# Kernel tuning notes

Measured on AMD Instinct MI355X. Metric: run time of the kernel, lower is better.

Reference implementation:

```python
import jax, jax.numpy as jnp
import numpy as np

B = 8192   # batch
N = 1024   # input feature dim
D = 64     # rotation dimension
K = D * (D - 1) // 2  # 2016 upper-triangular entries


def setup_inputs() -> dict:
    key = jax.random.key(0)
    k1, k2 = jax.random.split(key, 2)
    x = jax.random.normal(k1, (B, N), dtype=jnp.float32)
    # nn.Linear(N, K) parameters (kaiming-uniform-ish scale)
    W = jax.random.normal(k2, (K, N), dtype=jnp.float32) / np.float32(np.sqrt(N))
    b = jnp.zeros((K,), dtype=jnp.float32)
    return {"x": x, "W": W, "b": b}


def _skew_expm(A):
    # A is real skew-symmetric => iA is Hermitian: iA = V diag(w) V^H, w real.
    # Hence expm(A) = V diag(exp(-i w)) V^H, which is real orthogonal.
    # Mathematically identical to torch.linalg.matrix_exp(A).
    w, V = jnp.linalg.eigh(1j * A)              # complex64 eigh, batched
    R = jnp.einsum('bij,bj,bkj->bik', V, jnp.exp(-1j * w), V.conj())
    return jnp.real(R)


def reference(x, W, b):
    v = jax.nn.silu(x) @ W.T + b                # (B, K)
    iu, ju = jnp.triu_indices(D, k=1)           # strict upper triangle
    A = jnp.zeros((x.shape[0], D, D), v.dtype)
    A = A.at[:, iu, ju].set(v)
    A = A.at[:, ju, iu].set(-v)                 # skew-symmetric
    return _skew_expm(A)                        # (B, D, D)
```

## Files before the change

### kernel.cpp

```cpp
#include <hip/hip_runtime.h>
#include <hip/hip_bf16.h>
#include <hip/hip_fp16.h>
#include <math.h>

#define BB 8192
#define NF 1024
#define KKc 2016
#define DD 64

typedef unsigned short u16;
typedef __attribute__((ext_vector_type(4))) float f32x4;
typedef __attribute__((ext_vector_type(4))) unsigned int u32x4;
typedef __attribute__((ext_vector_type(8))) short s16x8;
typedef __attribute__((ext_vector_type(8))) _Float16 f16x8;
typedef __attribute__((ext_vector_type(8))) unsigned short u16x8;

union BF2U { __hip_bfloat162 b; unsigned u; };
union H2U { __half2 h; unsigned u; };
union F16U { s16x8 s; f16x8 h; };

__device__ __forceinline__ unsigned pk_hi(float a, float b, float& fa, float& fb) {
  BF2U r; r.b = __float22bfloat162_rn(make_float2(a, b));
  float2 f = __bfloat1622float2(r.b);
  fa = f.x; fb = f.y;
  return r.u;
}
__device__ __forceinline__ unsigned pk(float a, float b) {
  BF2U r; r.b = __float22bfloat162_rn(make_float2(a, b));
  return r.u;
}
__device__ __forceinline__ unsigned pkh(float a, float b) {
  H2U r; r.h = __float22half2_rn(make_float2(a, b));
  return r.u;
}

__device__ __forceinline__ void split4(const float t0, const float t1, const float t2,
                                       const float t3, uint2& h, uint2& l) {
  float f0, f1, f2, f3;
  h.x = pk_hi(t0, t1, f0, f1);
  h.y = pk_hi(t2, t3, f2, f3);
  l.x = pk(t0 - f0, t1 - f1);
  l.y = pk(t2 - f2, t3 - f3);
}

__global__ __launch_bounds__(256)
void silu_f16_kernel(const float* __restrict__ x, u16* __restrict__ xf) {
  const int idx = blockIdx.x * 256 + threadIdx.x;
  float4 vv = ((const float4*)x)[idx];
  float a[4] = {vv.x, vv.y, vv.z, vv.w};
#pragma unroll
  for (int i = 0; i < 4; i++) a[i] = a[i] / (1.f + __expf(-a[i]));
  uint2 o;
  o.x = pkh(a[0], a[1]);
  o.y = pkh(a[2], a[3]);
  ((uint2*)xf)[idx] = o;
}

__global__ __launch_bounds__(256)
void w_f16_kernel(const float* __restrict__ W, u16* __restrict__ wfp) {
  const int idx = blockIdx.x * 256 + threadIdx.x;
  const int row = idx >> 8;
  float4 vv = make_float4(0.f, 0.f, 0.f, 0.f);
  if (row < KKc) vv = ((const float4*)W)[idx];
  uint2 o;
  o.x = pkh(vv.x, vv.y);
  o.y = pkh(vv.z, vv.w);
  ((uint2*)wfp)[idx] = o;
}

typedef __attribute__((address_space(1))) const unsigned int gu32;
typedef __attribute__((address_space(3))) unsigned int lu32;

__device__ __forceinline__ void gload_lds16(const void* g, void* l) {
  __builtin_amdgcn_global_load_lds((gu32*)g, (lu32*)l, 16, 0, 0);
}

__device__ __forceinline__ s16x8 frag_row32(const u16* T, int row, int kc) {
  const int c = kc ^ ((row >> 1) & 3);
  return *(const s16x8*)(T + row * 32 + c * 8);
}

__global__ __launch_bounds__(256, 4)
void gemm_f16_kernel(const u16* __restrict__ xf, const u16* __restrict__ wfp,
                     const float* __restrict__ bias, float* __restrict__ v) {
  __shared__ __align__(16) u16 Af[128 * 32];
  __shared__ __align__(16) u16 Bf[128 * 32];
  const int tid = threadIdx.x;
  const int l = tid & 63, w = tid >> 6;
  const int wi = w >> 1, wj = w & 1;
  const int lin = (blockIdx.x & 7) * 128 + (blockIdx.x >> 3);
  const int n0 = (lin & 15) * 128;
  const int m0 = (lin >> 4) * 128;
  const int kc = l >> 4, lr = l & 15;

  const u16* P = (w < 2) ? xf : wfp;
  u16* T = (w < 2) ? Af : Bf;
  const int row0 = ((w < 2) ? m0 : n0) + (w & 1) * 64;
  u16* Th = T + (w & 1) * 2048;

  f32x4 acc[4][4];
  const f32x4 zz = {0.f, 0.f, 0.f, 0.f};
#pragma unroll
  for (int a = 0; a < 4; a++)
#pragma unroll
    for (int b = 0; b < 4; b++) acc[a][b] = zz;

  for (int k0 = 0; k0 < NF; k0 += 32) {
#pragma unroll
    for (int c4 = 0; c4 < 4; c4++) {
      const int slot = c4 * 64 + l;
      const int r = slot >> 2;
      const int c = (slot & 3) ^ ((r >> 1) & 3);
      gload_lds16(P + (size_t)(row0 + r) * NF + k0 + c * 8, Th + c4 * 512);
    }
    __syncthreads();

    F16U fa[4], fb[4];
#pragma unroll
    for (int a = 0; a < 4; a++) fa[a].s = frag_row32(Af, wi * 64 + a * 16 + lr, kc);
#pragma unroll
    for (int b = 0; b < 4; b++) fb[b].s = frag_row32(Bf, wj * 64 + b * 16 + lr, kc);
#pragma unroll
    for (int b = 0; b < 4; b++)
#pragma unroll
      for (int a = 0; a < 4; a++)
        acc[a][b] = __builtin_amdgcn_mfma_f32_16x16x32_f16(fa[a].h, fb[b].h, acc[a][b], 0, 0, 0);
    __syncthreads();
  }

  const int grp = l >> 4;
#pragma unroll
  for (int b = 0; b < 4; b++) {
    const int n = n0 + wj * 64 + b * 16 + lr;
    if (n < KKc) {
      const float bb = bias[n];
#pragma unroll
      for (int a = 0; a < 4; a++) {
        const int mbase = m0 + wi * 64 + a * 16 + grp * 4;
#pragma unroll
        for (int i = 0; i < 4; i++)
          v[(size_t)(mbase + i) * KKc + n] = acc[a][b][i] + bb;
      }
    }
  }
}

#define BM 128
#define BN 128
#define BKr 16
#define XST 132

__global__ __launch_bounds__(256, 2)
void gemm_silu_kernel(const float* __restrict__ x, const float* __restrict__ W,
                      const float* __restrict__ bias, float* __restrict__ v) {
  __shared__ float xs[BKr * XST];
  __shared__ float wl[BKr * XST];
  const int tid = threadIdx.x;
  const int tx = tid & 15, ty = tid >> 4;
  const int c0g = blockIdx.x * BN;
  const int m0 = blockIdx.y * BM;
  const int lrow = tid >> 2;
  const int lu = (tid & 3) << 2;

  float acc[2][2][4][4];
#pragma unroll
  for (int a = 0; a < 2; a++)
#pragma unroll
    for (int b = 0; b < 2; b++)
#pragma unroll
      for (int i = 0; i < 4; i++)
#pragma unroll
        for (int j = 0; j < 4; j++) acc[a][b][i][j] = 0.f;

  for (int n0 = 0; n0 < NF; n0 += BKr) {
#pragma unroll
    for (int p = 0; p < 2; p++) {
      const int row = lrow + 64 * p;
      float4 xv = *(const float4*)(x + (size_t)(m0 + row) * NF + n0 + lu);
      float xa[4] = {xv.x, xv.y, xv.z, xv.w};
#pragma unroll
      for (int u = 0; u < 4; u++) {
        const float val = xa[u];
        xs[(lu + u) * XST + row] = val / (1.f + __expf(-val));
      }
      const int wr = c0g + row;
      float4 wv = make_float4(0.f, 0.f, 0.f, 0.f);
      if (wr < KKc) wv = *(const float4*)(W + (size_t)wr * NF + n0 + lu);
      float wa[4] = {wv.x, wv.y, wv.z, wv.w};
#pragma unroll
      for (int u = 0; u < 4; u++) wl[(lu + u) * XST + row] = wa[u];
    }
    __syncthreads();
#pragma unroll
    for (int k0 = 0; k0 < BKr; k0 += 4) {
#pragma unroll
      for (int kk = 0; kk < 4; kk++) {
        const float* xr = xs + (k0 + kk) * XST;
        const float* wr_ = wl + (k0 + kk) * XST;
        float4 t;
        t = *(const float4*)(xr + 4 * ty);       float a0[4] = {t.x, t.y, t.z, t.w};
        t = *(const float4*)(xr + 64 + 4 * ty);  float a1[4] = {t.x, t.y, t.z, t.w};
        t = *(const float4*)(wr_ + 4 * tx);      float b0[4] = {t.x, t.y, t.z, t.w};
        t = *(const float4*)(wr_ + 64 + 4 * tx); float b1[4] = {t.x, t.y, t.z, t.w};
#pragma unroll
        for (int i = 0; i < 4; i++)
#pragma unroll
          for (int j = 0; j < 4; j++) {
            acc[0][0][i][j] = fmaf(a0[i], b0[j], acc[0][0][i][j]);
            acc[0][1][i][j] = fmaf(a0[i], b1[j], acc[0][1][i][j]);
            acc[1][0][i][j] = fmaf(a1[i], b0[j], acc[1][0][i][j]);
            acc[1][1][i][j] = fmaf(a1[i], b1[j], acc[1][1][i][j]);
          }
      }
    }
    __syncthreads();
  }
#pragma unroll
  for (int rb = 0; rb < 2; rb++)
#pragma unroll
    for (int ii = 0; ii < 4; ii++) {
      const int row = m0 + rb * 64 + 4 * ty + ii;
#pragma unroll
      for (int cb = 0; cb < 2; cb++) {
        const int c = c0g + cb * 64 + 4 * tx;
        if (c < KKc) {
          float4 bb = *(const float4*)(bias + c);
          float4 o;
          o.x = acc[rb][cb][ii][0] + bb.x;
          o.y = acc[rb][cb][ii][1] + bb.y;
          o.z = acc[rb][cb][ii][2] + bb.z;
          o.w = acc[rb][cb][ii][3] + bb.w;
          *(float4*)(v + (size_t)row * KKc + c) = o;
        }
      }
    }
}


__device__ __forceinline__ s16x8 fragld(const u16* P, int row, int chunk) {
  return *(const s16x8*)(P + ((row << 6) | ((chunk ^ (row & 7)) << 3)));
}

__device__ __forceinline__ void mat_mm3(const u16* APh, const u16* APl,
                                        const u16* BPh, const u16* BPl,
                                        f32x4 acc[2][2], int wi, int wj, int g, int lr) {
#pragma unroll
  for (int kb = 0; kb < 2; kb++) {
    const int ch = (kb << 2) | g;
    s16x8 bh[2], bl[2];
#pragma unroll
    for (int b = 0; b < 2; b++) {
      const int n = wj * 32 + b * 16 + lr;
      bh[b] = fragld(BPh, n, ch);
      bl[b] = fragld(BPl, n, ch);
    }
#pragma unroll
    for (int a = 0; a < 2; a++) {
      const int r = wi * 32 + a * 16 + lr;
      const s16x8 ah = fragld(APh, r, ch);
      const s16x8 al = fragld(APl, r, ch);
#pragma unroll
      for (int b = 0; b < 2; b++) {
        acc[a][b] = __builtin_amdgcn_mfma_f32_16x16x32_bf16(ah, bh[b], acc[a][b], 0, 0, 0);
        acc[a][b] = __builtin_amdgcn_mfma_f32_16x16x32_bf16(ah, bl[b], acc[a][b], 0, 0, 0);
        acc[a][b] = __builtin_amdgcn_mfma_f32_16x16x32_bf16(al, bh[b], acc[a][b], 0, 0, 0);
      }
    }
  }
}

__device__ __forceinline__ void mat_mm1h(const u16* AP, const u16* BP,
                                         f32x4 acc[2][2], int wi, int wj, int g, int lr) {
#pragma unroll
  for (int kb = 0; kb < 2; kb++) {
    const int ch = (kb << 2) | g;
    F16U bh[2];
#pragma unroll
    for (int b = 0; b < 2; b++) bh[b].s = fragld(BP, wj * 32 + b * 16 + lr, ch);
#pragma unroll
    for (int a = 0; a < 2; a++) {
      F16U ah; ah.s = fragld(AP, wi * 32 + a * 16 + lr, ch);
#pragma unroll
      for (int b = 0; b < 2; b++)
        acc[a][b] = __builtin_amdgcn_mfma_f32_16x16x32_f16(ah.h, bh[b].h, acc[a][b], 0, 0, 0);
    }
  }
}

__device__ __forceinline__ void pack_col(u16* Ch, u16* Cl, const f32x4 acc[2][2],
                                         int wi, int wj, int g, int lr) {
#pragma unroll
  for (int a = 0; a < 2; a++) {
    const int r0 = wi * 32 + a * 16 + g * 4;
#pragma unroll
    for (int b = 0; b < 2; b++) {
      const int c = wj * 32 + b * 16 + lr;
      uint2 h, l;
      split4(acc[a][b][0], acc[a][b][1], acc[a][b][2], acc[a][b][3], h, l);
      const int ad = (c << 6) | (((((r0 >> 3)) ^ (c & 7)) << 3) | (r0 & 7));
      *(uint2*)(Ch + ad) = h;
      *(uint2*)(Cl + ad) = l;
    }
  }
}

__device__ __forceinline__ void pack_colh(u16* C, const f32x4 acc[2][2], float sc,
                                          int wi, int wj, int g, int lr) {
#pragma unroll
  for (int a = 0; a < 2; a++) {
    const int r0 = wi * 32 + a * 16 + g * 4;
#pragma unroll
    for (int b = 0; b < 2; b++) {
      const int c = wj * 32 + b * 16 + lr;
      uint2 h;
      h.x = pkh(sc * acc[a][b][0], sc * acc[a][b][1]);
      h.y = pkh(sc * acc[a][b][2], sc * acc[a][b][3]);
      const int ad = (c << 6) | (((((r0 >> 3)) ^ (c & 7)) << 3) | (r0 & 7));
      *(uint2*)(C + ad) = h;
    }
  }
}

__device__ __forceinline__ void pack_dualh(u16* Rrow, u16* Rcol, const f32x4 acc[2][2],
                                           int wi, int wj, int g, int lr) {
#pragma unroll
  for (int a = 0; a < 2; a++) {
    const int r0 = wi * 32 + a * 16 + g * 4;
#pragma unroll
    for (int b = 0; b < 2; b++) {
      const int c = wj * 32 + b * 16 + lr;
      uint2 h;
      h.x = pkh(acc[a][b][0], acc[a][b][1]);
      h.y = pkh(acc[a][b][2], acc[a][b][3]);
      const int adc = (c << 6) | (((((r0 >> 3)) ^ (c & 7)) << 3) | (r0 & 7));
      *(uint2*)(Rcol + adc) = h;
      const u16 hv[4] = {(u16)h.x, (u16)(h.x >> 16), (u16)h.y, (u16)(h.y >> 16)};
#pragma unroll
      for (int i = 0; i < 4; i++) {
        const int r = r0 + i;
        const int adr = (r << 6) | ((((c >> 3) ^ (r & 7)) << 3) | (c & 7));
        Rrow[adr] = hv[i];
      }
    }
  }
}

__global__ __launch_bounds__(256, 4)
void expm_kernel(const float* __restrict__ v, float* __restrict__ out,
                 float* __restrict__ redg) {
  __shared__ __align__(16) u16 PAh[4096], PAl[4096];
  __shared__ __align__(16) u16 PF2[4096], PF4[4096];
  const int tid = threadIdx.x;
  const int bid = blockIdx.x;
  const int l = tid & 63, w = tid >> 6;
  const int g = l >> 4, lr = l & 15;
  const int wi = w >> 1, wj = w & 1;

  {
    float* vb = (float*)PF2;
    const float* vr = v + (size_t)bid * KKc;
    for (int i = tid; i < KKc; i += 256) vb[i] = vr[i];
  }
  __syncthreads();

  {
    const float* vb = (const float*)PF2;
    const int arow = tid >> 2, q = tid & 3;
    float va[16];
#pragma unroll
    for (int j = 0; j < 16; j++) {
      const int c = q * 16 + j;
      float val = 0.f;
      if (arow < c)      val =  vb[(arow * (127 - arow)) / 2 + c - arow - 1];
      else if (arow > c) val = -vb[(c * (127 - c)) / 2 + arow - c - 1];
      va[j] = val;
    }
#pragma unroll
    for (int cc = 0; cc < 2; cc++) {
      const int ch = 2 * q + cc;
      const int ad = (arow << 6) | ((ch ^ (arow & 7)) << 3);
      unsigned hw[4], lw[4], fw[4];
#pragma unroll
      for (int p = 0; p < 4; p++) {
        const float a = va[cc * 8 + 2 * p], b = va[cc * 8 + 2 * p + 1];
        float fa, fb;
        hw[p] = pk_hi(a, b, fa, fb);
        lw[p] = pk(a - fa, b - fb);
        fw[p] = pkh(a, b);
      }
      *(u32x4*)(PAh + ad) = (u32x4){hw[0], hw[1], hw[2], hw[3]};
      *(u32x4*)(PAl + ad) = (u32x4){lw[0], lw[1], lw[2], lw[3]};
      *(u32x4*)(PF4 + ad) = (u32x4){fw[0], fw[1], fw[2], fw[3]};
    }
  }
  __syncthreads();

  const f32x4 zz = {0.f, 0.f, 0.f, 0.f};
  f32x4 acc[2][2];

  acc[0][0] = zz; acc[0][1] = zz; acc[1][0] = zz; acc[1][1] = zz;
  mat_mm1h(PF4, PF4, acc, wi, wj, g, lr);
  f32x4 rM[2][2];
  rM[0][0] = acc[0][0]; rM[0][1] = acc[0][1]; rM[1][0] = acc[1][0]; rM[1][1] = acc[1][1];
  {
    float fs = 0.f;
#pragma unroll
    for (int a = 0; a < 2; a++)
#pragma unroll
      for (int b = 0; b < 2; b++)
#pragma unroll
        for (int i = 0; i < 4; i++) fs = fmaf(rM[a][b][i], rM[a][b][i], fs);
#pragma unroll
    for (int k = 1; k < 64; k <<= 1) fs += __shfl_xor(fs, k, 64);
    if (l == 0) ((float*)PF2)[w] = fs;
  }
  __syncthreads();

  const float* redA = (const float*)PF2;
  const float nf4 = redA[0] + redA[1] + redA[2] + redA[3];
  int s0 = 0;
  if (nf4 > 1.f) {
    s0 = (int)ceilf(0.25f * log2f(nf4));
    if (s0 < 0) s0 = 0;
    if (s0 > 15) s0 = 15;
  }
  const float t0 = exp2f(-(float)s0);

  pack_colh(PF4, rM, -(t0 * t0), wi, wj, g, lr);
  __syncthreads();

  acc[0][0] = zz; acc[0][1] = zz; acc[1][0] = zz; acc[1][1] = zz;
  mat_mm1h(PF4, PF4, acc, wi, wj, g, lr);
  {
    float fs = 0.f;
#pragma unroll
    for (int a = 0; a < 2; a++)
#pragma unroll
      for (int b = 0; b < 2; b++)
#pragma unroll
        for (int i = 0; i < 4; i++) fs = fmaf(acc[a][b][i], acc[a][b][i], fs);
#pragma unroll
    for (int k = 1; k < 64; k <<= 1) fs += __shfl_xor(fs, k, 64);
    if (l == 0) redg[bid * 4 + w] = fs;
  }
  pack_colh(PF2, acc, 1.f, wi, wj, g, lr);
  __syncthreads();

  const float nf8 = redg[bid * 4 + 0] + redg[bid * 4 + 1]
                  + redg[bid * 4 + 2] + redg[bid * 4 + 3];
  int s = 0;
  if (nf8 > 1e-30f) {
    s = (int)ceilf(0.125f * log2f(nf8) + (float)s0 - 1.0f);
    if (s < 0) s = 0;
    if (s > 15) s = 15;
  }
  const float t = exp2f(-(float)s);
  const float r = exp2f((float)(s0 - s));
  const float r2 = r * r, r4 = r2 * r2, r6 = r4 * r2, r8 = r4 * r4;
  const float t2 = t * t;

  f32x4 rE[2][2], rS3[2][2];
#pragma unroll
  for (int a = 0; a < 2; a++)
#pragma unroll
    for (int b = 0; b < 2; b++)
#pragma unroll
      for (int i = 0; i < 4; i++) {
        const int row = wi * 32 + a * 16 + g * 4 + i;
        const int col = wj * 32 + b * 16 + lr;
        const float dg = (row == col) ? 1.f : 0.f;
        rE[a][b][i]  = dg - (0.5f * t2) * rM[a][b][i] + (r4 / 24.f) * acc[a][b][i];
        rS3[a][b][i] = t * dg - (t * t2 / 6.f) * rM[a][b][i]
                             + (t * r4 / 120.f) * acc[a][b][i];
      }

  acc[0][0] = zz; acc[0][1] = zz; acc[1][0] = zz; acc[1][1] = zz;
  mat_mm1h(PF2, PF4, acc, wi, wj, g, lr);
#pragma unroll
  for (int a = 0; a < 2; a++)
#pragma unroll
    for (int b = 0; b < 2; b++)
#pragma unroll
      for (int i = 0; i < 4; i++) {
        rE[a][b][i]  += (r6 / 720.f) * acc[a][b][i];
        rS3[a][b][i] += (t * r6 / 5040.f) * acc[a][b][i];
      }
  acc[0][0] = zz; acc[0][1] = zz; acc[1][0] = zz; acc[1][1] = zz;
  mat_mm1h(PF2, PF2, acc, wi, wj, g, lr);
#pragma unroll
  for (int a = 0; a < 2; a++)
#pragma unroll
    for (int b = 0; b < 2; b++)
#pragma unroll
      for (int i = 0; i < 4; i++) {
        rE[a][b][i]  += (r8 / 40320.f) * acc[a][b][i];
        rS3[a][b][i] += (t * r8 / 362880.f) * acc[a][b][i];
      }
  __syncthreads();

  pack_col(PF4, PF2, rS3, wi, wj, g, lr);
  __syncthreads();

  acc[0][0] = rE[0][0]; acc[0][1] = rE[0][1]; acc[1][0] = rE[1][0]; acc[1][1] = rE[1][1];
  mat_mm3(PAh, PAl, PF4, PF2, acc, wi, wj, g, lr);
  __syncthreads();

  for (int it = 0; it < s; it++) {
    u16* Rrow = (it & 1) ? PF2 : PAl;
    u16* Rcol = (it & 1) ? PF4 : PAh;
    pack_dualh(Rrow, Rcol, acc, wi, wj, g, lr);
    __syncthreads();
    acc[0][0] = zz; acc[0][1] = zz; acc[1][0] = zz; acc[1][1] = zz;
    mat_mm1h(Rrow, Rcol, acc, wi, wj, g, lr);
  }

  float* ob = out + (size_t)bid * 4096;
#pragma unroll
  for (int a = 0; a < 2; a++)
#pragma unroll
    for (int b = 0; b < 2; b++)
#pragma unroll
      for (int i = 0; i < 4; i++) {
        const int row = wi * 32 + a * 16 + g * 4 + i;
        const int col = wj * 32 + b * 16 + lr;
        ob[row * 64 + col] = acc[a][b][i];
      }
}

extern "C" void kernel_launch(void* const* d_in, const int* in_sizes, int n_in,
                              void* d_out, int out_size, void* d_ws, size_t ws_size,
                              hipStream_t stream) {
  const float* x = (const float*)d_in[0];
  const float* W = (const float*)d_in[1];
  const float* bias = (const float*)d_in[2];
  float* out = (float*)d_out;
  char* ws = (char*)d_ws;
  float* v = (float*)ws;

  const size_t V_BYTES  = (size_t)BB * KKc * 4;
  const size_t XF_ELEMS = (size_t)BB * NF;
  const size_t WF_ELEMS = (size_t)2048 * NF;
  const size_t NEED = V_BYTES + (XF_ELEMS + WF_ELEMS) * 2;
  float* redg = (float*)(ws + V_BYTES);

  if (ws_size >= NEED) {
    u16* xf = (u16*)(ws + V_BYTES);
    u16* wfp = xf + XF_ELEMS;
    silu_f16_kernel<<<dim3(BB * NF / 4 / 256), dim3(256), 0, stream>>>(x, xf);
    w_f16_kernel<<<dim3(2048 * NF / 4 / 256), dim3(256), 0, stream>>>(W, wfp);
    gemm_f16_kernel<<<dim3(1024), dim3(256), 0, stream>>>(xf, wfp, bias, v);
  } else {
    dim3 g1((KKc + BN - 1) / BN, BB / BM);
    gemm_silu_kernel<<<g1, dim3(256), 0, stream>>>(x, W, bias, v);
  }
  expm_kernel<<<dim3(BB), dim3(256), 0, stream>>>(v, out, redg);
}
```

Before: 167.1 us.

## Fix expm prescale, drop norm reduction, merge prep kernels, raise occupancy

The expm kernel no longer computes the first Frobenius-norm reduction and its extra barrier to choose a per-matrix prescale s0. Instead it always scales A^2 by 1/16 and folds the matching powers of 4 into the Taylor coefficients. The skew-matrix assembly now uses incrementally updated triangular indices, and launch bounds go from 4 to 5 blocks per CU. The silu and W fp16 conversion kernels are merged into one launch. The fixed prescale assumes matrix norms stay in a range where the fp16 intermediates neither overflow nor lose accuracy, and higher occupancy may squeeze registers.

New measurement: 170.1 us. No clear change (+1.8%).

```diff
diff --git a/kernel.cpp b/kernel.cpp
--- a/kernel.cpp
+++ b/kernel.cpp
@@ -44,28 +44,29 @@
 }
 
 __global__ __launch_bounds__(256)
-void silu_f16_kernel(const float* __restrict__ x, u16* __restrict__ xf) {
-  const int idx = blockIdx.x * 256 + threadIdx.x;
-  float4 vv = ((const float4*)x)[idx];
-  float a[4] = {vv.x, vv.y, vv.z, vv.w};
-#pragma unroll
-  for (int i = 0; i < 4; i++) a[i] = a[i] / (1.f + __expf(-a[i]));
-  uint2 o;
-  o.x = pkh(a[0], a[1]);
-  o.y = pkh(a[2], a[3]);
-  ((uint2*)xf)[idx] = o;
-}
-
-__global__ __launch_bounds__(256)
-void w_f16_kernel(const float* __restrict__ W, u16* __restrict__ wfp) {
-  const int idx = blockIdx.x * 256 + threadIdx.x;
-  const int row = idx >> 8;
-  float4 vv = make_float4(0.f, 0.f, 0.f, 0.f);
-  if (row < KKc) vv = ((const float4*)W)[idx];
-  uint2 o;
-  o.x = pkh(vv.x, vv.y);
-  o.y = pkh(vv.z, vv.w);
-  ((uint2*)wfp)[idx] = o;
+void prep_f16_kernel(const float* __restrict__ x, const float* __restrict__ W,
+                     u16* __restrict__ xf, u16* __restrict__ wfp) {
+  const int bid = blockIdx.x;
+  if (bid < BB) {
+    const int idx = bid * 256 + threadIdx.x;
+    float4 vv = ((const float4*)x)[idx];
+    float a[4] = {vv.x, vv.y, vv.z, vv.w};
+#pragma unroll
+    for (int i = 0; i < 4; i++) a[i] = a[i] / (1.f + __expf(-a[i]));
+    uint2 o;
+    o.x = pkh(a[0], a[1]);
+    o.y = pkh(a[2], a[3]);
+    ((uint2*)xf)[idx] = o;
+  } else {
+    const int idx = (bid - BB) * 256 + threadIdx.x;
+    const int row = idx >> 8;
+    float4 vv = make_float4(0.f, 0.f, 0.f, 0.f);
+    if (row < KKc) vv = ((const float4*)W)[idx];
+    uint2 o;
+    o.x = pkh(vv.x, vv.y);
+    o.y = pkh(vv.z, vv.w);
+    ((uint2*)wfp)[idx] = o;
+  }
 }
 
 typedef __attribute__((address_space(1))) const unsigned int gu32;
@@ -345,11 +346,11 @@
   }
 }
 
-__global__ __launch_bounds__(256, 4)
+__global__ __launch_bounds__(256, 5)
 void expm_kernel(const float* __restrict__ v, float* __restrict__ out,
                  float* __restrict__ redg) {
-  __shared__ __align__(16) u16 PAh[4096], PAl[4096];
-  __shared__ __align__(16) u16 PF2[4096], PF4[4096];
+  __shared__ __align__(16) u16 P0[4096], P1[4096];
+  __shared__ __align__(16) u16 P2[4096], P3[4096];
   const int tid = threadIdx.x;
   const int bid = blockIdx.x;
   const int l = tid & 63, w = tid >> 6;
@@ -357,23 +358,27 @@
   const int wi = w >> 1, wj = w & 1;
 
   {
-    float* vb = (float*)PF2;
+    float* vb = (float*)P2;
     const float* vr = v + (size_t)bid * KKc;
     for (int i = tid; i < KKc; i += 256) vb[i] = vr[i];
   }
   __syncthreads();
 
   {
-    const float* vb = (const float*)PF2;
+    const float* vb = (const float*)P2;
     const int arow = tid >> 2, q = tid & 3;
+    const int ub = (arow * (127 - arow)) / 2 - arow - 1;
+    const int c0 = q * 16;
+    int il = (c0 * (127 - c0)) / 2 + arow - c0 - 1;
     float va[16];
 #pragma unroll
     for (int j = 0; j < 16; j++) {
-      const int c = q * 16 + j;
+      const int c = c0 + j;
       float val = 0.f;
-      if (arow < c)      val =  vb[(arow * (127 - arow)) / 2 + c - arow - 1];
-      else if (arow > c) val = -vb[(c * (127 - c)) / 2 + arow - c - 1];
+      if (arow < c)      val =  vb[ub + c];
+      else if (arow > c) val = -vb[il];
       va[j] = val;
+      il += 62 - c;
     }
 #pragma unroll
     for (int cc = 0; cc < 2; cc++) {
@@ -388,9 +393,9 @@
         lw[p] = pk(a - fa, b - fb);
         fw[p] = pkh(a, b);
       }
-      *(u32x4*)(PAh + ad) = (u32x4){hw[0], hw[1], hw[2], hw[3]};
-      *(u32x4*)(PAl + ad) = (u32x4){lw[0], lw[1], lw[2], lw[3]};
-      *(u32x4*)(PF4 + ad) = (u32x4){fw[0], fw[1], fw[2], fw[3]};
+      *(u32x4*)(P0 + ad) = (u32x4){hw[0], hw[1], hw[2], hw[3]};
+      *(u32x4*)(P1 + ad) = (u32x4){lw[0], lw[1], lw[2], lw[3]};
+      *(u32x4*)(P3 + ad) = (u32x4){fw[0], fw[1], fw[2], fw[3]};
     }
   }
   __syncthreads();
@@ -399,9 +404,14 @@
   f32x4 acc[2][2];
 
   acc[0][0] = zz; acc[0][1] = zz; acc[1][0] = zz; acc[1][1] = zz;
-  mat_mm1h(PF4, PF4, acc, wi, wj, g, lr);
+  mat_mm1h(P3, P3, acc, wi, wj, g, lr);
   f32x4 rM[2][2];
   rM[0][0] = acc[0][0]; rM[0][1] = acc[0][1]; rM[1][0] = acc[1][0]; rM[1][1] = acc[1][1];
+  pack_colh(P2, rM, -0.0625f, wi, wj, g, lr);
+  __syncthreads();
+
+  acc[0][0] = zz; acc[0][1] = zz; acc[1][0] = zz; acc[1][1] = zz;
+  mat_mm1h(P2, P2, acc, wi, wj, g, lr);
   {
     float fs = 0.f;
 #pragma unroll
@@ -409,55 +419,29 @@
 #pragma unroll
       for (int b = 0; b < 2; b++)
 #pragma unroll
-        for (int i = 0; i < 4; i++) fs = fmaf(rM[a][b][i], rM[a][b][i], fs);
-#pragma unroll
-    for (int k = 1; k < 64; k <<= 1) fs += __shfl_xor(fs, k, 64);
-    if (l == 0) ((float*)PF2)[w] = fs;
-  }
-  __syncthreads();
-
-  const float* redA = (const float*)PF2;
-  const float nf4 = redA[0] + redA[1] + redA[2] + redA[3];
-  int s0 = 0;
-  if (nf4 > 1.f) {
-    s0 = (int)ceilf(0.25f * log2f(nf4));
-    if (s0 < 0) s0 = 0;
-    if (s0 > 15) s0 = 15;
-  }
-  const float t0 = exp2f(-(float)s0);
-
-  pack_colh(PF4, rM, -(t0 * t0), wi, wj, g, lr);
-  __syncthreads();
-
-  acc[0][0] = zz; acc[0][1] = zz; acc[1][0] = zz; acc[1][1] = zz;
-  mat_mm1h(PF4, PF4, acc, wi, wj, g, lr);
-  {
-    float fs = 0.f;
-#pragma unroll
-    for (int a = 0; a < 2; a++)
-#pragma unroll
-      for (int b = 0; b < 2; b++)
-#pragma unroll
         for (int i = 0; i < 4; i++) fs = fmaf(acc[a][b][i], acc[a][b][i], fs);
 #pragma unroll
     for (int k = 1; k < 64; k <<= 1) fs += __shfl_xor(fs, k, 64);
     if (l == 0) redg[bid * 4 + w] = fs;
   }
-  pack_colh(PF2, acc, 1.f, wi, wj, g, lr);
+  pack_colh(P3, acc, 1.f, wi, wj, g, lr);
   __syncthreads();
 
   const float nf8 = redg[bid * 4 + 0] + redg[bid * 4 + 1]
                   + redg[bid * 4 + 2] + redg[bid * 4 + 3];
   int s = 0;
   if (nf8 > 1e-30f) {
-    s = (int)ceilf(0.125f * log2f(nf8) + (float)s0 - 1.0f);
+    s = (int)ceilf(1.0f + 0.125f * log2f(nf8));
     if (s < 0) s = 0;
     if (s > 15) s = 15;
   }
   const float t = exp2f(-(float)s);
-  const float r = exp2f((float)(s0 - s));
-  const float r2 = r * r, r4 = r2 * r2, r6 = r4 * r2, r8 = r4 * r4;
-  const float t2 = t * t;
+  const float t2 = t * t, t4 = t2 * t2, t6 = t4 * t2, t8 = t4 * t4;
+  const float e2 = 0.5f * t2,            e4 = 256.f * t4 / 24.f;
+  const float e6 = 4096.f * t6 / 720.f,  e8 = 65536.f * t8 / 40320.f;
+  const float o1 = t,                    o3 = t * t2 / 6.f;
+  const float o5 = 256.f * t * t4 / 120.f, o7 = 4096.f * t * t6 / 5040.f;
+  const float o9 = 65536.f * t * t8 / 362880.f;
 
   f32x4 rE[2][2], rS3[2][2];
 #pragma unroll
@@ -469,45 +453,44 @@
         const int row = wi * 32 + a * 16 + g * 4 + i;
         const int col = wj * 32 + b * 16 + lr;
         const float dg = (row == col) ? 1.f : 0.f;
-        rE[a][b][i]  = dg - (0.5f * t2) * rM[a][b][i] + (r4 / 24.f) * acc[a][b][i];
-        rS3[a][b][i] = t * dg - (t * t2 / 6.f) * rM[a][b][i]
-                             + (t * r4 / 120.f) * acc[a][b][i];
+        rE[a][b][i]  = dg - e2 * rM[a][b][i] + e4 * acc[a][b][i];
+        rS3[a][b][i] = o1 * dg - o3 * rM[a][b][i] + o5 * acc[a][b][i];
       }
 
   acc[0][0] = zz; acc[0][1] = zz; acc[1][0] = zz; acc[1][1] = zz;
-  mat_mm1h(PF2, PF4, acc, wi, wj, g, lr);
+  mat_mm1h(P3, P2, acc, wi, wj, g, lr);
 #pragma unroll
   for (int a = 0; a < 2; a++)
 #pragma unroll
     for (int b = 0; b < 2; b++)
 #pragma unroll
       for (int i = 0; i < 4; i++) {
-        rE[a][b][i]  += (r6 / 720.f) * acc[a][b][i];
-        rS3[a][b][i] += (t * r6 / 5040.f) * acc[a][b][i];
+        rE[a][b][i]  += e6 * acc[a][b][i];
+        rS3[a][b][i] += o7 * acc[a][b][i];
       }
   acc[0][0] = zz; acc[0][1] = zz; acc[1][0] = zz; acc[1][1] = zz;
-  mat_mm1h(PF2, PF2, acc, wi, wj, g, lr);
+  mat_mm1h(P3, P3, acc, wi, wj, g, lr);
 #pragma unroll
   for (int a = 0; a < 2; a++)
 #pragma unroll
     for (int b = 0; b < 2; b++)
 #pragma unroll
       for (int i = 0; i < 4; i++) {
-        rE[a][b][i]  += (r8 / 40320.f) * acc[a][b][i];
-        rS3[a][b][i] += (t * r8 / 362880.f) * acc[a][b][i];
-      }
-  __syncthreads();
-
-  pack_col(PF4, PF2, rS3, wi, wj, g, lr);
+        rE[a][b][i]  += e8 * acc[a][b][i];
+        rS3[a][b][i] += o9 * acc[a][b][i];
+      }
+  __syncthreads();
+
+  pack_col(P2, P3, rS3, wi, wj, g, lr);
   __syncthreads();
 
   acc[0][0] = rE[0][0]; acc[0][1] = rE[0][1]; acc[1][0] = rE[1][0]; acc[1][1] = rE[1][1];
-  mat_mm3(PAh, PAl, PF4, PF2, acc, wi, wj, g, lr);
+  mat_mm3(P0, P1, P2, P3, acc, wi, wj, g, lr);
   __syncthreads();
 
   for (int it = 0; it < s; it++) {
-    u16* Rrow = (it & 1) ? PF2 : PAl;
-    u16* Rcol = (it & 1) ? PF4 : PAh;
+    u16* Rrow = (it & 1) ? P3 : P1;
+    u16* Rcol = (it & 1) ? P2 : P0;
     pack_dualh(Rrow, Rcol, acc, wi, wj, g, lr);
     __syncthreads();
     acc[0][0] = zz; acc[0][1] = zz; acc[1][0] = zz; acc[1][1] = zz;
@@ -546,8 +529,7 @@
   if (ws_size >= NEED) {
     u16* xf = (u16*)(ws + V_BYTES);
     u16* wfp = xf + XF_ELEMS;
-    silu_f16_kernel<<<dim3(BB * NF / 4 / 256), dim3(256), 0, stream>>>(x, xf);
-    w_f16_kernel<<<dim3(2048 * NF / 4 / 256), dim3(256), 0, stream>>>(W, wfp);
+    prep_f16_kernel<<<dim3(BB + 2048), dim3(256), 0, stream>>>(x, W, xf, wfp);
     gemm_f16_kernel<<<dim3(1024), dim3(256), 0, stream>>>(xf, wfp, bias, v);
   } else {
     dim3 g1((KKc + BN - 1) / BN, BB / BM);
```
